# Optimization experiments

Measured on AMD Instinct MI355X. Metric: run time of the kernel, lower is better.

## Reference

```python
import jax, jax.numpy as jnp
import numpy as np

B, T, D, H = 32, 512, 512, 512


def setup_inputs() -> dict:
    key = jax.random.key(0)
    ks = jax.random.split(key, 10)
    s = 1.0 / np.sqrt(H)
    def u(k, shape):
        return jax.random.uniform(k, shape, jnp.float32, -s, s)
    return {
        "x": jax.random.normal(ks[0], (B, T, D), jnp.float32),
        "lengths": jax.random.randint(ks[1], (B,), 1, T + 1, jnp.int32),
        "W_ih_f": u(ks[2], (4 * H, D)),
        "W_hh_f": u(ks[3], (4 * H, H)),
        "b_ih_f": u(ks[4], (4 * H,)),
        "b_hh_f": u(ks[5], (4 * H,)),
        "W_ih_b": u(ks[6], (4 * H, D)),
        "W_hh_b": u(ks[7], (4 * H, H)),
        "b_ih_b": u(ks[8], (4 * H,)),
        "b_hh_b": u(ks[9], (4 * H,)),
    }


def _lstm_scan(x, mask, W_ih, W_hh, b_ih, b_hh, reverse):
    # Precompute input projections for all timesteps: [T, B, 4H]
    xg = jnp.einsum('btd,gd->tbg', x, W_ih) + b_ih + b_hh
    h0 = jnp.zeros((x.shape[0], H), x.dtype)
    c0 = jnp.zeros((x.shape[0], H), x.dtype)

    def step(carry, inp):
        h, c = carry
        xg_t, m = inp  # xg_t: [B,4H], m: [B,1]
        gates = xg_t + h @ W_hh.T
        i, f, g, o = jnp.split(gates, 4, axis=-1)
        i, f, o = jax.nn.sigmoid(i), jax.nn.sigmoid(f), jax.nn.sigmoid(o)
        g = jnp.tanh(g)
        c_new = f * c + i * g
        h_new = o * jnp.tanh(c_new)
        h = m * h_new + (1.0 - m) * h
        c = m * c_new + (1.0 - m) * c
        return (h, c), h

    (_, _), hs = jax.lax.scan(step, (h0, c0), (xg, mask), reverse=reverse)
    return hs.transpose(1, 0, 2)  # [B,T,H]


def reference(x, lengths, W_ih_f, W_hh_f, b_ih_f, b_hh_f, W_ih_b, W_hh_b, b_ih_b, b_hh_b):
    Tn = x.shape[1]
    # mask[t,b,1] = lengths[b] > t ; padded steps hold previous state
    mask = (lengths[None, :] > jnp.arange(Tn)[:, None]).astype(x.dtype)[:, :, None]
    fwd = _lstm_scan(x, mask, W_ih_f, W_hh_f, b_ih_f, b_hh_f, reverse=False)
    bwd = _lstm_scan(x, mask, W_ih_b, W_hh_b, b_ih_b, b_hh_b, reverse=True)
    return jnp.concatenate([fwd, bwd], axis=-1)  # [B,T,2H]
```

## Files before the change

kernel.cpp:

```cpp
#include <hip/hip_runtime.h>
#include <hip/hip_cooperative_groups.h>

namespace cg = cooperative_groups;


#define Bv 32
#define Tv 512
#define Dv 512
#define Hv 512
#define XS 520
#define HS 520
#define PUN 16896

__device__ __forceinline__ float sigmf_(float x) { return 1.0f / (1.0f + __expf(-x)); }
__device__ __forceinline__ float tanhf_(float x) { return 2.0f / (1.0f + __expf(-2.0f * x)) - 1.0f; }

__global__ __launch_bounds__(512, 2) void bilstm_coop5(
    const float* __restrict__ x, const int* __restrict__ lengths,
    const float* __restrict__ Wih_f, const float* __restrict__ Whh_f,
    const float* __restrict__ bih_f, const float* __restrict__ bhh_f,
    const float* __restrict__ Wih_b, const float* __restrict__ Whh_b,
    const float* __restrict__ bih_b, const float* __restrict__ bhh_b,
    float* __restrict__ out, unsigned int* __restrict__ cnt)
{
    __shared__ float xb[8 * XS];
    __shared__ float hu[PUN];
    __shared__ float gates[64 * 9];
    __shared__ float bias_s[64];

    const int tid  = threadIdx.x;
    const int w    = blockIdx.x;

    const int xcd    = w & 7;
    const int slot   = w >> 3;
    const int dir    = xcd >> 2;
    const int cslice = (xcd & 3) * 8 + (slot & 7);
    const int bg     = slot >> 3;
    const int c0     = cslice * 16;
    const int b0     = bg * 8;
    const int group  = dir * 4 + bg;

    unsigned int* myslot = cnt + (size_t)group * 64 + cslice;

    const float* Wih = dir ? Wih_b : Wih_f;
    const float* Whh = dir ? Whh_b : Whh_f;
    const float* bih = dir ? bih_b : bih_f;
    const float* bhh = dir ? bhh_b : bhh_f;

    if (tid == 0)
        __hip_atomic_store(myslot, 0u, __ATOMIC_RELAXED, __HIP_MEMORY_SCOPE_AGENT);
    if (tid < 64) {
        int g = tid >> 4, cell = tid & 15;
        int rg = g * Hv + c0 + cell;
        bias_s[tid] = bih[rg] + bhh[rg];
    }
    cg::this_grid().sync();

    const int pos  = tid >> 5;
    const int kseg = tid & 31;

    int wrow[4];
    #pragma unroll
    for (int i = 0; i < 4; ++i) {
        int r = pos * 4 + i;
        wrow[i] = (r >> 4) * Hv + c0 + (r & 15);
    }

    float4 whr[4][4];
    #pragma unroll
    for (int j = 0; j < 4; ++j)
        #pragma unroll
        for (int i = 0; i < 4; ++i)
            whr[j][i] = *(const float4*)(Whh + (size_t)wrow[i] * Dv
                                             + (j * 32 + kseg) * 4);

    const int pw_ib   = tid >> 4;
    const int pw_cell = tid & 15;
    float cst_r = 0.0f;
    int   len_r = 0;
    if (tid < 128) len_r = lengths[b0 + pw_ib];

    for (int s = 0; s < Tv; ++s) {
        const int t = dir ? (Tv - 1 - s) : s;

        #pragma unroll
        for (int j = 0; j < 2; ++j) {
            int F  = tid + j * 512;
            int bl = F >> 7, cf = F & 127;
            *(float4*)(xb + bl * XS + cf * 4) =
                *(const float4*)(x + ((size_t)(b0 + bl) * Tv + t) * Dv + cf * 4);
        }
        __syncthreads();

        float acc[4][8];
        #pragma unroll
        for (int i = 0; i < 4; ++i)
            #pragma unroll
            for (int ib = 0; ib < 8; ++ib) acc[i][ib] = 0.0f;

        #pragma unroll
        for (int j = 0; j < 4; ++j) {
            const int col = (j * 32 + kseg) * 4;
            float4 wv[4];
            #pragma unroll
            for (int i = 0; i < 4; ++i)
                wv[i] = *(const float4*)(Wih + (size_t)wrow[i] * Dv + col);
            float4 xv[8];
            #pragma unroll
            for (int ib = 0; ib < 8; ++ib)
                xv[ib] = *(const float4*)(xb + ib * XS + col);
            #pragma unroll
            for (int i = 0; i < 4; ++i)
                #pragma unroll
                for (int ib = 0; ib < 8; ++ib)
                    acc[i][ib] += wv[i].x * xv[ib].x + wv[i].y * xv[ib].y
                                + wv[i].z * xv[ib].z + wv[i].w * xv[ib].w;
        }

        if (s > 0 && tid < 32) {
            const unsigned int tgt = (unsigned int)s;
            const unsigned int* sl = cnt + (size_t)group * 64 + tid;
            while (__hip_atomic_load(sl, __ATOMIC_RELAXED,
                                     __HIP_MEMORY_SCOPE_AGENT) < tgt)
                __builtin_amdgcn_s_sleep(1);
        }
        __syncthreads();

        if (s == 0) {
            #pragma unroll
            for (int j = 0; j < 2; ++j) {
                int F  = tid + j * 512;
                int bl = F >> 7, cf = F & 127;
                *(float4*)(hu + bl * HS + cf * 4) = make_float4(0.f, 0.f, 0.f, 0.f);
            }
        } else {
            const int tp = dir ? (t + 1) : (t - 1);
            #pragma unroll
            for (int j = 0; j < 2; ++j) {
                int F  = tid + j * 512;
                int bl = F >> 7, cf = F & 127;
                *(float4*)(hu + bl * HS + cf * 4) =
                    *(const float4*)(out + ((size_t)(b0 + bl) * Tv + tp) * (2 * Hv)
                                         + dir * Hv + cf * 4);
            }
        }
        __syncthreads();

        float hpv = 0.0f;
        if (tid < 128) hpv = hu[pw_ib * HS + c0 + pw_cell];

        #pragma unroll
        for (int j = 0; j < 4; ++j) {
            const int col = (j * 32 + kseg) * 4;
            float4 hv[8];
            #pragma unroll
            for (int ib = 0; ib < 8; ++ib)
                hv[ib] = *(const float4*)(hu + ib * HS + col);
            #pragma unroll
            for (int i = 0; i < 4; ++i)
                #pragma unroll
                for (int ib = 0; ib < 8; ++ib)
                    acc[i][ib] += whr[j][i].x * hv[ib].x + whr[j][i].y * hv[ib].y
                                + whr[j][i].z * hv[ib].z + whr[j][i].w * hv[ib].w;
        }
        __syncthreads();

        float* part = hu;
        #pragma unroll
        for (int i = 0; i < 4; ++i) {
            const int r = pos * 4 + i;
            #pragma unroll
            for (int ib = 0; ib < 8; ++ib)
                part[(r * 8 + ib) * 33 + kseg] = acc[i][ib];
        }
        __syncthreads();

        {
            const float* pr = part + tid * 33;
            float s0 = 0.f, s1 = 0.f, s2 = 0.f, s3 = 0.f;
            #pragma unroll
            for (int m = 0; m < 32; m += 4) {
                s0 += pr[m + 0]; s1 += pr[m + 1]; s2 += pr[m + 2]; s3 += pr[m + 3];
            }
            gates[(tid >> 3) * 9 + (tid & 7)] =
                ((s0 + s1) + (s2 + s3)) + bias_s[tid >> 3];
        }
        __syncthreads();

        if (tid < 128) {
            float gi = sigmf_(gates[( 0 + pw_cell) * 9 + pw_ib]);
            float gf = sigmf_(gates[(16 + pw_cell) * 9 + pw_ib]);
            float gg = tanhf_(gates[(32 + pw_cell) * 9 + pw_ib]);
            float go = sigmf_(gates[(48 + pw_cell) * 9 + pw_ib]);
            float cn = gf * cst_r + gi * gg;
            float hn = go * tanhf_(cn);
            const bool v = (t < len_r);
            float ho = v ? hn : hpv;
            cst_r = v ? cn : cst_r;
            __hip_atomic_store(out + ((size_t)(b0 + pw_ib) * Tv + t) * (2 * Hv)
                                   + dir * Hv + c0 + pw_cell,
                               ho, __ATOMIC_RELAXED, __HIP_MEMORY_SCOPE_AGENT);
        }
        __syncthreads();

        if (tid == 0)
            __hip_atomic_store(myslot, (unsigned int)(s + 1),
                               __ATOMIC_RELEASE, __HIP_MEMORY_SCOPE_AGENT);
    }
}

__global__ __launch_bounds__(1024, 1) void bilstm_simple(
    const float* __restrict__ x,
    const int* __restrict__ lengths,
    const float* __restrict__ Wih_f, const float* __restrict__ Whh_f,
    const float* __restrict__ bih_f, const float* __restrict__ bhh_f,
    const float* __restrict__ Wih_b, const float* __restrict__ Whh_b,
    const float* __restrict__ bih_b, const float* __restrict__ bhh_b,
    float* __restrict__ out)
{
    __shared__ float xh[Dv + Hv];
    __shared__ float cst[Hv];
    __shared__ float gates[4 * Hv];
    __shared__ float bias[4 * Hv];

    const int tid  = threadIdx.x;
    const int wave = tid >> 6;
    const int lane = tid & 63;
    const int dir  = blockIdx.x >> 5;
    const int b    = blockIdx.x & 31;

    const float* Wih = dir ? Wih_b : Wih_f;
    const float* Whh = dir ? Whh_b : Whh_f;
    const float* bih = dir ? bih_b : bih_f;
    const float* bhh = dir ? bhh_b : bhh_f;

    for (int i = tid; i < 4 * Hv; i += 1024) bias[i] = bih[i] + bhh[i];
    for (int i = tid; i < Hv; i += 1024) { xh[Dv + i] = 0.f; cst[i] = 0.f; }
    const int len = lengths[b];

    const float* Wbase = (lane < 32) ? Wih : Whh;
    const int koff = (lane & 31) * 16;

    for (int s = 0; s < Tv; ++s) {
        const int t = dir ? (Tv - 1 - s) : s;
        __syncthreads();
        for (int i = tid; i < Dv; i += 1024)
            xh[i] = x[((size_t)b * Tv + t) * Dv + i];
        __syncthreads();

        float4 xr0 = *(const float4*)(xh + lane * 16 + 0);
        float4 xr1 = *(const float4*)(xh + lane * 16 + 4);
        float4 xr2 = *(const float4*)(xh + lane * 16 + 8);
        float4 xr3 = *(const float4*)(xh + lane * 16 + 12);

        #pragma unroll 4
        for (int rr = 0; rr < 128; ++rr) {
            const int row = wave * 128 + rr;
            const float4* wr = (const float4*)(Wbase + (size_t)row * 512 + koff);
            const float4 w0 = wr[0], w1 = wr[1], w2 = wr[2], w3 = wr[3];
            float acc = w0.x * xr0.x + w0.y * xr0.y + w0.z * xr0.z + w0.w * xr0.w
                      + w1.x * xr1.x + w1.y * xr1.y + w1.z * xr1.z + w1.w * xr1.w
                      + w2.x * xr2.x + w2.y * xr2.y + w2.z * xr2.z + w2.w * xr2.w
                      + w3.x * xr3.x + w3.y * xr3.y + w3.z * xr3.z + w3.w * xr3.w;
            #pragma unroll
            for (int off = 32; off > 0; off >>= 1)
                acc += __shfl_xor(acc, off, 64);
            if (lane == 0) gates[row] = acc;
        }
        __syncthreads();

        if (tid < Hv) {
            const int cc = tid;
            const float gi = sigmf_(gates[0 * Hv + cc] + bias[0 * Hv + cc]);
            const float gf = sigmf_(gates[1 * Hv + cc] + bias[1 * Hv + cc]);
            const float gg = tanhf_(gates[2 * Hv + cc] + bias[2 * Hv + cc]);
            const float go = sigmf_(gates[3 * Hv + cc] + bias[3 * Hv + cc]);
            const float cn = gf * cst[cc] + gi * gg;
            const float hn = go * tanhf_(cn);
            const bool v = (t < len);
            const float hnew = v ? hn : xh[Dv + cc];
            cst[cc] = v ? cn : cst[cc];
            xh[Dv + cc] = hnew;
            out[((size_t)b * Tv + t) * (2 * Hv) + dir * Hv + cc] = hnew;
        }
    }
}

extern "C" void kernel_launch(void* const* d_in, const int* in_sizes, int n_in,
                              void* d_out, int out_size, void* d_ws, size_t ws_size,
                              hipStream_t stream) {
    (void)out_size;

    const void *xv, *len_p, *Wihf, *Whhf, *bihf, *bhhf, *Wihb, *Whhb, *bihb, *bhhb;
    if (n_in == 10 && in_sizes[9] == 8388608 && in_sizes[8] == 32) {
        Whhb = d_in[0]; Whhf = d_in[1]; Wihb = d_in[2]; Wihf = d_in[3];
        bhhb = d_in[4]; bhhf = d_in[5]; bihb = d_in[6]; bihf = d_in[7];
        len_p = d_in[8]; xv = d_in[9];
    } else {
        xv = d_in[0]; len_p = d_in[1];
        Wihf = d_in[2]; Whhf = d_in[3]; bihf = d_in[4]; bhhf = d_in[5];
        Wihb = d_in[6]; Whhb = d_in[7]; bihb = d_in[8]; bhhb = d_in[9];
    }

    const float* xf  = (const float*)xv;
    const int*   lp  = (const int*)len_p;
    const float* wif = (const float*)Wihf;  const float* whf = (const float*)Whhf;
    const float* bif = (const float*)bihf;  const float* bhf = (const float*)bhhf;
    const float* wib = (const float*)Wihb;  const float* whb = (const float*)Whhb;
    const float* bib = (const float*)bihb;  const float* bhb = (const float*)bhhb;
    float* outp = (float*)d_out;
    unsigned int* cntp = (unsigned int*)d_ws;

    if (ws_size >= 8 * 64 * sizeof(unsigned int)) {
        void* args[12] = { &xf, &lp, &wif, &whf, &bif, &bhf,
                           &wib, &whb, &bib, &bhb, &outp, &cntp };
        hipError_t e = hipLaunchCooperativeKernel((const void*)bilstm_coop5,
                                                  dim3(256), dim3(512),
                                                  args, 0, stream);
        if (e == hipSuccess) return;
    }

    bilstm_simple<<<dim3(64), dim3(1024), 0, stream>>>(
        xf, lp, wif, whf, bif, bhf, wib, whb, bib, bhb, outp);
}
```

Before: 5.366 ms.

## Co-locate recurrence groups per XCD, spin on L2-scoped loads, shuffle-reduce partials

Remaps blocks so that every block in one direction/batch-group recurrence shares a single XCD (group = xcd). The intent is that per-step flag polling and h exchange stay within one L2. The spin-wait now uses a custom L2-level (sc0) load, with an occasional agent-scope atomic fallback. The partial-sum reduction is reworked: wave shuffles first combine groups of four k-segments, which shrinks the shared-memory scratch and the serial summation. The risks are coherence correctness, since the sc0 loads and plain output stores rely on same-XCD L2 sharing, and that the XCD-to-block mapping assumption (w&7) may not hold.

```diff
diff --git a/kernel.cpp b/kernel.cpp
--- a/kernel.cpp
+++ b/kernel.cpp
@@ -10,12 +10,20 @@
 #define Hv 512
 #define XS 520
 #define HS 520
-#define PUN 16896
+#define PUN 4608
 
 __device__ __forceinline__ float sigmf_(float x) { return 1.0f / (1.0f + __expf(-x)); }
 __device__ __forceinline__ float tanhf_(float x) { return 2.0f / (1.0f + __expf(-2.0f * x)) - 1.0f; }
 
-__global__ __launch_bounds__(512, 2) void bilstm_coop5(
+__device__ __forceinline__ unsigned int l2_load_u32(const unsigned int* p) {
+    unsigned int v;
+    asm volatile("global_load_dword %0, %1, off sc0\n\t"
+                 "s_waitcnt vmcnt(0)"
+                 : "=v"(v) : "v"(p) : "memory");
+    return v;
+}
+
+__global__ __launch_bounds__(512, 2) void bilstm_coop10(
     const float* __restrict__ x, const int* __restrict__ lengths,
     const float* __restrict__ Wih_f, const float* __restrict__ Whh_f,
     const float* __restrict__ bih_f, const float* __restrict__ bhh_f,
@@ -28,17 +36,16 @@
     __shared__ float gates[64 * 9];
     __shared__ float bias_s[64];
 
-    const int tid  = threadIdx.x;
-    const int w    = blockIdx.x;
+    const int tid = threadIdx.x;
+    const int w   = blockIdx.x;
 
     const int xcd    = w & 7;
-    const int slot   = w >> 3;
     const int dir    = xcd >> 2;
-    const int cslice = (xcd & 3) * 8 + (slot & 7);
-    const int bg     = slot >> 3;
+    const int bg     = xcd & 3;
+    const int cslice = w >> 3;
     const int c0     = cslice * 16;
     const int b0     = bg * 8;
-    const int group  = dir * 4 + bg;
+    const int group  = xcd;
 
     unsigned int* myslot = cnt + (size_t)group * 64 + cslice;
 
@@ -47,11 +54,13 @@
     const float* bih = dir ? bih_b : bih_f;
     const float* bhh = dir ? bhh_b : bhh_f;
 
-    if (tid == 0)
+    if (tid == 0) {
+        *(volatile unsigned int*)myslot = 0u;
         __hip_atomic_store(myslot, 0u, __ATOMIC_RELAXED, __HIP_MEMORY_SCOPE_AGENT);
+    }
     if (tid < 64) {
-        int g = tid >> 4, cell = tid & 15;
-        int rg = g * Hv + c0 + cell;
+        int gate = tid >> 4, cell = tid & 15;
+        int rg = gate * Hv + c0 + cell;
         bias_s[tid] = bih[rg] + bhh[rg];
     }
     cg::this_grid().sync();
@@ -80,6 +89,8 @@
     int   len_r = 0;
     if (tid < 128) len_r = lengths[b0 + pw_ib];
 
+    float* part = hu;
+
     for (int s = 0; s < Tv; ++s) {
         const int t = dir ? (Tv - 1 - s) : s;
 
@@ -120,9 +131,17 @@
         if (s > 0 && tid < 32) {
             const unsigned int tgt = (unsigned int)s;
             const unsigned int* sl = cnt + (size_t)group * 64 + tid;
-            while (__hip_atomic_load(sl, __ATOMIC_RELAXED,
-                                     __HIP_MEMORY_SCOPE_AGENT) < tgt)
+            int spins = 0;
+            for (;;) {
+                unsigned int v = l2_load_u32(sl);
+                if (v >= tgt) break;
+                if ((++spins & 63) == 0) {
+                    v = __hip_atomic_load(sl, __ATOMIC_RELAXED,
+                                          __HIP_MEMORY_SCOPE_AGENT);
+                    if (v >= tgt) break;
+                }
                 __builtin_amdgcn_s_sleep(1);
+            }
         }
         __syncthreads();
 
@@ -165,47 +184,55 @@
         }
         __syncthreads();
 
-        float* part = hu;
-        #pragma unroll
-        for (int i = 0; i < 4; ++i) {
-            const int r = pos * 4 + i;
-            #pragma unroll
-            for (int ib = 0; ib < 8; ++ib)
-                part[(r * 8 + ib) * 33 + kseg] = acc[i][ib];
+        #pragma unroll
+        for (int i = 0; i < 4; ++i)
+            #pragma unroll
+            for (int ib = 0; ib < 8; ++ib) {
+                float v = acc[i][ib];
+                v += __shfl_xor(v, 1, 64);
+                v += __shfl_xor(v, 2, 64);
+                acc[i][ib] = v;
+            }
+        if ((kseg & 3) == 0) {
+            const int q = kseg >> 2;
+            #pragma unroll
+            for (int i = 0; i < 4; ++i) {
+                const int r = pos * 4 + i;
+                #pragma unroll
+                for (int ib = 0; ib < 8; ++ib)
+                    part[(r * 8 + ib) * 9 + q] = acc[i][ib];
+            }
         }
         __syncthreads();
 
         {
-            const float* pr = part + tid * 33;
-            float s0 = 0.f, s1 = 0.f, s2 = 0.f, s3 = 0.f;
-            #pragma unroll
-            for (int m = 0; m < 32; m += 4) {
-                s0 += pr[m + 0]; s1 += pr[m + 1]; s2 += pr[m + 2]; s3 += pr[m + 3];
-            }
-            gates[(tid >> 3) * 9 + (tid & 7)] =
-                ((s0 + s1) + (s2 + s3)) + bias_s[tid >> 3];
+            const float* pr = part + tid * 9;
+            float s0 = (pr[0] + pr[1]) + (pr[2] + pr[3]);
+            float s1 = (pr[4] + pr[5]) + (pr[6] + pr[7]);
+            gates[(tid >> 3) * 9 + (tid & 7)] = s0 + s1 + bias_s[tid >> 3];
         }
         __syncthreads();
 
         if (tid < 128) {
-            float gi = sigmf_(gates[( 0 + pw_cell) * 9 + pw_ib]);
-            float gf = sigmf_(gates[(16 + pw_cell) * 9 + pw_ib]);
-            float gg = tanhf_(gates[(32 + pw_cell) * 9 + pw_ib]);
-            float go = sigmf_(gates[(48 + pw_cell) * 9 + pw_ib]);
+            float gi = sigmf_(gates[(0 * 16 + pw_cell) * 9 + pw_ib]);
+            float gf = sigmf_(gates[(1 * 16 + pw_cell) * 9 + pw_ib]);
+            float gg = tanhf_(gates[(2 * 16 + pw_cell) * 9 + pw_ib]);
+            float go = sigmf_(gates[(3 * 16 + pw_cell) * 9 + pw_ib]);
             float cn = gf * cst_r + gi * gg;
             float hn = go * tanhf_(cn);
-            const bool v = (t < len_r);
-            float ho = v ? hn : hpv;
-            cst_r = v ? cn : cst_r;
-            __hip_atomic_store(out + ((size_t)(b0 + pw_ib) * Tv + t) * (2 * Hv)
-                                   + dir * Hv + c0 + pw_cell,
-                               ho, __ATOMIC_RELAXED, __HIP_MEMORY_SCOPE_AGENT);
-        }
-        __syncthreads();
-
-        if (tid == 0)
+            const bool vld = (t < len_r);
+            float ho = vld ? hn : hpv;
+            cst_r = vld ? cn : cst_r;
+            out[((size_t)(b0 + pw_ib) * Tv + t) * (2 * Hv) + dir * Hv + c0 + pw_cell]
+                = ho;
+        }
+        __syncthreads();
+
+        if (tid == 0) {
+            *(volatile unsigned int*)myslot = (unsigned int)(s + 1);
             __hip_atomic_store(myslot, (unsigned int)(s + 1),
                                __ATOMIC_RELEASE, __HIP_MEMORY_SCOPE_AGENT);
+        }
     }
 }
 
@@ -314,7 +341,7 @@
     if (ws_size >= 8 * 64 * sizeof(unsigned int)) {
         void* args[12] = { &xf, &lp, &wif, &whf, &bif, &bhf,
                            &wib, &whb, &bib, &bhb, &outp, &cntp };
-        hipError_t e = hipLaunchCooperativeKernel((const void*)bilstm_coop5,
+        hipError_t e = hipLaunchCooperativeKernel((const void*)bilstm_coop10,
                                                   dim3(256), dim3(512),
                                                   args, 0, stream);
         if (e == hipSuccess) return;
```

New measurement: 9.890 ms. 1.84x slower.
